# Performance work log

Measured on AMD Instinct MI355X. Metric: run time of the kernel, lower is better.

Reference implementation:

```python
import jax, jax.numpy as jnp
import numpy as np

VIEW_NUM = 360
CHAN_NUM = 512
BATCH = 2
IMG = 512


def setup_inputs() -> dict:
    key = jax.random.key(0)
    x = jax.random.normal(key, (BATCH, 1, IMG, IMG), dtype=jnp.float32)
    return {"x": x}


def _bilinear_sample_zeros(img, ix, iy):
    """Bilinear sample img (B,1,H,W) at pixel coords ix, iy (H,W), zeros padding.
    Matches F.grid_sample(mode='bilinear', padding_mode='zeros', align_corners=False)."""
    H, W = img.shape[-2], img.shape[-1]
    x0 = jnp.floor(ix)
    y0 = jnp.floor(iy)
    x1 = x0 + 1.0
    y1 = y0 + 1.0
    wx1 = ix - x0
    wx0 = 1.0 - wx1
    wy1 = iy - y0
    wy0 = 1.0 - wy1

    def gather(yy, xx):
        valid = (xx >= 0) & (xx <= W - 1) & (yy >= 0) & (yy <= H - 1)
        xi = jnp.clip(xx, 0, W - 1).astype(jnp.int32)
        yi = jnp.clip(yy, 0, H - 1).astype(jnp.int32)
        # fancy-index over spatial dims -> (B,1,H,W)
        return img[:, :, yi, xi] * valid.astype(img.dtype)

    return (gather(y0, x0) * (wy0 * wx0)
            + gather(y0, x1) * (wy0 * wx1)
            + gather(y1, x0) * (wy1 * wx0)
            + gather(y1, x1) * (wy1 * wx1))


def _fp(x):
    B, C, H, W = x.shape
    # affine_grid base coords, align_corners=False: (2i+1)/N - 1
    bx = (2.0 * jnp.arange(W, dtype=x.dtype) + 1.0) / W - 1.0
    by = (2.0 * jnp.arange(H, dtype=x.dtype) + 1.0) / H - 1.0
    X = bx[None, :]  # (1,W)
    Y = by[:, None]  # (H,1)
    i = jnp.arange(VIEW_NUM, dtype=x.dtype)
    angles = -jnp.pi * (i + 1.0) / VIEW_NUM - jnp.pi
    cosv = jnp.cos(angles)
    sinv = jnp.sin(angles)

    def per_view(carry, cs):
        c, s = cs
        # theta = [[c,-s,0],[s,c,0]]; grid = base @ theta^T
        gx = c * X - s * Y  # (H,W) normalized sample x
        gy = s * X + c * Y  # (H,W) normalized sample y
        # unnormalize (align_corners=False)
        ix = ((gx + 1.0) * W - 1.0) * 0.5
        iy = ((gy + 1.0) * H - 1.0) * 0.5
        samp = _bilinear_sample_zeros(x, ix, iy)  # (B,1,H,W)
        return carry, jnp.sum(samp, axis=2)  # sum over height -> (B,1,W)

    _, cols = jax.lax.scan(per_view, 0, (cosv, sinv))  # (V,B,1,W)
    sino = jnp.transpose(cols, (1, 2, 3, 0)) * 0.5  # (B,1,chanNum,viewNum)
    return sino


def reference(x):
    return _fp(x)
```

## Files before the change

kernel.cpp:

```cpp
#include <hip/hip_runtime.h>

typedef __fp16 h2 __attribute__((ext_vector_type(2)));

constexpr int VIEWS = 360;
constexpr int IMGSZ = 512;
constexpr int WCHUNK = 64;
constexpr int KH = 64;
constexpr int PITCH = 101;
constexpr int MAXNY = 94;
constexpr int LDSDW = PITCH * MAXNY;
constexpr int PW = 712;
constexpr int PH = 704;
constexpr int PAD = 96;
constexpr int RJOBS = 96;
constexpr int KJOBS = 25;
constexpr int NIT = (RJOBS * KJOBS + 255) / 256;

__global__ __launch_bounds__(256) void pad_kernel(const float* __restrict__ x,
                                                  unsigned* __restrict__ padq) {
    constexpr int PW4 = PW / 4;
    constexpr int total = PH * PW4;
    int idx = blockIdx.x * 256 + threadIdx.x;
    if (idx >= total) return;
    int py = idx / PW4;
    int px4 = idx - py * PW4;
    int gx = px4 * 4 - PAD;
    int gy = py - PAD;
    const float* img0 = x;
    const float* img1 = x + (size_t)IMGSZ * IMGSZ;
    float4 a = make_float4(0.f, 0.f, 0.f, 0.f);
    float4 bq = a;
    if ((unsigned)gy < (unsigned)IMGSZ && (unsigned)gx < (unsigned)IMGSZ) {
        size_t off = (size_t)gy * IMGSZ + gx;
        a  = *(const float4*)(img0 + off);
        bq = *(const float4*)(img1 + off);
    }
    uint4 d;
    d.x = __builtin_bit_cast(unsigned, __builtin_amdgcn_cvt_pkrtz(a.x, bq.x));
    d.y = __builtin_bit_cast(unsigned, __builtin_amdgcn_cvt_pkrtz(a.y, bq.y));
    d.z = __builtin_bit_cast(unsigned, __builtin_amdgcn_cvt_pkrtz(a.z, bq.z));
    d.w = __builtin_bit_cast(unsigned, __builtin_amdgcn_cvt_pkrtz(a.w, bq.w));
    *(uint4*)&padq[(size_t)idx * 4] = d;
}

__global__ __launch_bounds__(256, 4) void fp_kernel(const unsigned* __restrict__ padq,
                                                    float* __restrict__ out) {
    __shared__ __align__(16) unsigned tileU[LDSDW];

    int blk = blockIdx.x;
    int wc = blk & 7;
    int v = blk >> 3;

    int tid = threadIdx.x;
    int lane = tid & 63;
    int g = tid >> 6;
    int w = wc * WCHUNK + lane;

    double ang = -3.14159265358979323846 * (double)(v + 1) / (double)VIEWS
                 - 3.14159265358979323846;
    float c = (float)cos(ang);
    float s = (float)sin(ang);

    float xw = (float)w + 0.5f - 256.0f;
    float cxw = fmaf(c, xw, 255.5f);
    float sxw = fmaf(s, xw, 255.5f);

    float lo = -1e30f, hi = 1e30f;
    {
        float coef = -s, base = cxw;
        if (fabsf(coef) > 1e-6f) {
            float a = (-1.0f - base) / coef;
            float bq = (512.0f - base) / coef;
            lo = fmaxf(lo, fminf(a, bq));
            hi = fminf(hi, fmaxf(a, bq));
        } else if (!(base > -1.0f && base < 512.0f)) {
            lo = 1e30f; hi = -1e30f;
        }
    }
    {
        float coef = c, base = sxw;
        if (fabsf(coef) > 1e-6f) {
            float a = (-1.0f - base) / coef;
            float bq = (512.0f - base) / coef;
            lo = fmaxf(lo, fminf(a, bq));
            hi = fminf(hi, fmaxf(a, bq));
        } else if (!(base > -1.0f && base < 512.0f)) {
            lo = 1e30f; hi = -1e30f;
        }
    }
    float h0f = fminf(fmaxf(floorf(lo + 255.5f) - 1.0f, 0.0f), 512.0f);
    float h1f = fminf(fmaxf(ceilf(hi + 255.5f) + 1.0f, -1.0f), 511.0f);
    int h0 = (int)h0f;
    int h1 = (int)h1f;

    int bh0 = h0, bh1 = h1;
    #pragma unroll
    for (int m = 1; m < 64; m <<= 1) {
        bh0 = min(bh0, __shfl_xor(bh0, m, 64));
        bh1 = max(bh1, __shfl_xor(bh1, m, 64));
    }

    float xa = (float)(wc * WCHUNK) + 0.5f - 256.0f;
    float xb = xa + 63.0f;

    float acc0 = 0.0f, acc1 = 0.0f;
    float step4x = -4.0f * s;
    float step4y = 4.0f * c;

    for (int hc = bh0; hc <= bh1; hc += KH) {
        int hend = min(hc + KH - 1, bh1);

        float ha = (float)hc - 255.5f;
        float hb = (float)hend - 255.5f;
        float ix00 = c * xa - s * ha, ix01 = c * xa - s * hb;
        float ix10 = c * xb - s * ha, ix11 = c * xb - s * hb;
        float iy00 = s * xa + c * ha, iy01 = s * xa + c * hb;
        float iy10 = s * xb + c * ha, iy11 = s * xb + c * hb;
        float ixmn = fminf(fminf(ix00, ix01), fminf(ix10, ix11)) + 255.5f;
        float iymn = fminf(fminf(iy00, iy01), fminf(iy10, iy11)) + 255.5f;
        float iymx = fmaxf(fmaxf(iy00, iy01), fmaxf(iy10, iy11)) + 255.5f;
        int x_lo = (int)floorf(ixmn) - 1;
        int x_lo4 = x_lo & ~3;
        int y_lo = (int)floorf(iymn) - 1;
        int NY = min((int)floorf(iymx) + 3 - y_lo, MAXNY);

        __syncthreads();

        {
            const unsigned* pb = padq + (y_lo + PAD) * PW + (x_lo4 + PAD);
            uint4 vals[NIT];
            #pragma unroll
            for (int it = 0; it < NIT; ++it) {
                int j = min(it * 256 + tid, RJOBS * KJOBS - 1);
                int k = j / RJOBS;
                int r = j - k * RJOBS;
                int rr = min(r, NY - 1);
                vals[it] = *(const uint4*)(pb + rr * PW + (k << 2));
            }
            #pragma unroll
            for (int it = 0; it < NIT; ++it) {
                int j = min(it * 256 + tid, RJOBS * KJOBS - 1);
                int k = j / RJOBS;
                int r = j - k * RJOBS;
                int rr = min(r, NY - 1);
                int base = rr * PITCH + (k << 2);
                tileU[base + 0] = vals[it].x;
                tileU[base + 1] = vals[it].y;
                tileU[base + 2] = vals[it].z;
                tileU[base + 3] = vals[it].w;
            }
        }
        __syncthreads();

        float hh0 = (float)(hc + g) - 255.5f;
        float ixr = fmaf(-s, hh0, cxw) - (float)x_lo4;
        float iyr = fmaf(c, hh0, sxw) - (float)y_lo;
        h2 accp0 = (h2)0.0f;
        h2 accp1 = (h2)0.0f;
        int parity = 0;
        #pragma unroll 8
        for (int h = hc + g; h <= hend; h += 4) {
            int lx = (int)ixr;
            int ly = (int)iyr;
            float wx1 = __builtin_amdgcn_fractf(ixr);
            float wy1 = __builtin_amdgcn_fractf(iyr);
            h2 wxs = __builtin_amdgcn_cvt_pkrtz(wx1, wx1);
            h2 wys = __builtin_amdgcn_cvt_pkrtz(wy1, wy1);
            const unsigned* p = tileU + (ly * PITCH + lx);
            h2 t00 = __builtin_bit_cast(h2, p[0]);
            h2 t01 = __builtin_bit_cast(h2, p[1]);
            h2 t10 = __builtin_bit_cast(h2, p[PITCH]);
            h2 t11 = __builtin_bit_cast(h2, p[PITCH + 1]);
            h2 r0 = t00 + (t01 - t00) * wxs;
            h2 r1 = t10 + (t11 - t10) * wxs;
            h2 contrib = r0 + (r1 - r0) * wys;
            if (parity) accp1 += contrib; else accp0 += contrib;
            parity ^= 1;
            ixr += step4x;
            iyr += step4y;
        }
        acc0 += (float)accp0.x + (float)accp1.x;
        acc1 += (float)accp0.y + (float)accp1.y;
    }

    __syncthreads();
    tileU[(g << 6) + lane] = __float_as_uint(acc0);
    tileU[256 + (g << 6) + lane] = __float_as_uint(acc1);
    __syncthreads();
    if (g == 0) {
        float r0 = __uint_as_float(tileU[lane]) + __uint_as_float(tileU[64 + lane]) +
                   __uint_as_float(tileU[128 + lane]) + __uint_as_float(tileU[192 + lane]);
        float r1 = __uint_as_float(tileU[256 + lane]) + __uint_as_float(tileU[320 + lane]) +
                   __uint_as_float(tileU[384 + lane]) + __uint_as_float(tileU[448 + lane]);
        size_t o = (size_t)w * VIEWS + v;
        out[o] = r0 * 0.5f;
        out[(size_t)IMGSZ * VIEWS + o] = r1 * 0.5f;
    }
}

extern "C" void kernel_launch(void* const* d_in, const int* in_sizes, int n_in,
                              void* d_out, int out_size, void* d_ws, size_t ws_size,
                              hipStream_t stream) {
    const float* x = (const float*)d_in[0];
    float* out = (float*)d_out;
    unsigned* padq = (unsigned*)d_ws;

    constexpr int padTotal = PH * (PW / 4);
    pad_kernel<<<(padTotal + 255) / 256, 256, 0, stream>>>(x, padq);

    int nblocks = VIEWS * (IMGSZ / WCHUNK);
    fp_kernel<<<nblocks, 256, 0, stream>>>(padq, out);
}
```

Before: 152.6 us.

## Restructure LDS tile fill per row and compute LDS address in float

The tile fill now assigns each row to two threads that stream twelve or thirteen consecutive 16-byte chunks, loading the next chunk while storing the current one. This replaces the flat job index with its integer divide and clamp, and skips rows beyond NY. In the inner sampling loop, truncf plus subtraction replaces the int conversion and fract, and the LDS byte offset is computed with one float FMA (row pitch 404 bytes) before a single conversion. The row-based mapping leaves threads with r >= NY idle and has a longer serial load chain per thread. The float address math relies on offsets staying exactly representable in float.

```diff
diff --git a/kernel.cpp b/kernel.cpp
--- a/kernel.cpp
+++ b/kernel.cpp
@@ -12,9 +12,6 @@
 constexpr int PW = 712;
 constexpr int PH = 704;
 constexpr int PAD = 96;
-constexpr int RJOBS = 96;
-constexpr int KJOBS = 25;
-constexpr int NIT = (RJOBS * KJOBS + 255) / 256;
 
 __global__ __launch_bounds__(256) void pad_kernel(const float* __restrict__ x,
                                                   unsigned* __restrict__ padq) {
@@ -56,6 +53,9 @@
     int g = tid >> 6;
     int w = wc * WCHUNK + lane;
 
+    int r = tid & 127;
+    int b = tid >> 7;
+
     double ang = -3.14159265358979323846 * (double)(v + 1) / (double)VIEWS
                  - 3.14159265358979323846;
     float c = (float)cos(ang);
@@ -126,28 +126,29 @@
 
         __syncthreads();
 
-        {
-            const unsigned* pb = padq + (y_lo + PAD) * PW + (x_lo4 + PAD);
-            uint4 vals[NIT];
+        if (r < NY) {
+            const unsigned* src = padq + (y_lo + PAD + r) * PW
+                                       + (x_lo4 + PAD) + (b << 2);
+            int dst = r * PITCH + (b << 2);
+            uint4 cur = *(const uint4*)src;
             #pragma unroll
-            for (int it = 0; it < NIT; ++it) {
-                int j = min(it * 256 + tid, RJOBS * KJOBS - 1);
-                int k = j / RJOBS;
-                int r = j - k * RJOBS;
-                int rr = min(r, NY - 1);
-                vals[it] = *(const uint4*)(pb + rr * PW + (k << 2));
+            for (int it = 0; it < 12; ++it) {
+                uint4 nxt;
+                if (it < 11 || b == 0)
+                    nxt = *(const uint4*)(src + 8 * (it + 1));
+                int d = dst + (it << 3);
+                tileU[d]     = cur.x;
+                tileU[d + 1] = cur.y;
+                tileU[d + 2] = cur.z;
+                tileU[d + 3] = cur.w;
+                cur = nxt;
             }
-            #pragma unroll
-            for (int it = 0; it < NIT; ++it) {
-                int j = min(it * 256 + tid, RJOBS * KJOBS - 1);
-                int k = j / RJOBS;
-                int r = j - k * RJOBS;
-                int rr = min(r, NY - 1);
-                int base = rr * PITCH + (k << 2);
-                tileU[base + 0] = vals[it].x;
-                tileU[base + 1] = vals[it].y;
-                tileU[base + 2] = vals[it].z;
-                tileU[base + 3] = vals[it].w;
+            if (b == 0) {
+                int d = dst + (12 << 3);
+                tileU[d]     = cur.x;
+                tileU[d + 1] = cur.y;
+                tileU[d + 2] = cur.z;
+                tileU[d + 3] = cur.w;
             }
         }
         __syncthreads();
@@ -160,13 +161,14 @@
         int parity = 0;
         #pragma unroll 8
         for (int h = hc + g; h <= hend; h += 4) {
-            int lx = (int)ixr;
-            int ly = (int)iyr;
-            float wx1 = __builtin_amdgcn_fractf(ixr);
-            float wy1 = __builtin_amdgcn_fractf(iyr);
+            float tx = truncf(ixr);
+            float ty = truncf(iyr);
+            float wx1 = ixr - tx;
+            float wy1 = iyr - ty;
             h2 wxs = __builtin_amdgcn_cvt_pkrtz(wx1, wx1);
             h2 wys = __builtin_amdgcn_cvt_pkrtz(wy1, wy1);
-            const unsigned* p = tileU + (ly * PITCH + lx);
+            unsigned a = (unsigned)fmaf(ty, 404.0f, tx * 4.0f);
+            const unsigned* p = (const unsigned*)((const char*)tileU + a);
             h2 t00 = __builtin_bit_cast(h2, p[0]);
             h2 t01 = __builtin_bit_cast(h2, p[1]);
             h2 t10 = __builtin_bit_cast(h2, p[PITCH]);
```

New measurement: 155.4 us. About the same (+1.8%).
